# Performance work log

Hardware: AMD Instinct MI355X
Metric: run time of the kernel (lower is better)

The kernel has to match this reference:

```python
import jax, jax.numpy as jnp
import numpy as np

KERNEL = 5
STRIDE = 1
D = 32
B = 8
L = 2048


def setup_inputs() -> dict:
    key = jax.random.key(0)
    k1, k2, k3, k4, k5 = jax.random.split(key, 5)
    dd = D * D
    scale_dense = 1.0 / np.sqrt(dd)
    scale_attn = 1.0 / np.sqrt(dd * KERNEL)
    return {
        "inputs": jax.random.normal(k1, (B, L, D, D), dtype=jnp.float32),
        "W_dense": jax.random.normal(k2, (dd, dd), dtype=jnp.float32) * scale_dense,
        "b_dense": jax.random.normal(k3, (dd,), dtype=jnp.float32) * scale_dense,
        "W_attn": jax.random.normal(k4, (KERNEL, dd * KERNEL), dtype=jnp.float32) * scale_attn,
        "b_attn": jax.random.normal(k5, (KERNEL,), dtype=jnp.float32) * scale_attn,
    }


def _forward(inputs, W_dense, b_dense, W_attn, b_attn):
    b, l, d, _ = inputs.shape
    pad = KERNEL - 1
    pad_left, pad_right = pad // 2, (pad - 1) // 2 + 1

    # Linear2D: linear over flattened d*d dims
    h = jnp.einsum('blde,fe->bldf',
                   inputs.reshape(b, l, d * d)[..., None, :].squeeze(-2).reshape(b, l, 1, d * d),
                   W_dense).reshape(b, l, d * d) + b_dense
    h = h.reshape(b, l, d, d)

    # pad_identity: pad seq dim with identity matrices (neutral for matrix chain)
    eye = jnp.broadcast_to(jnp.eye(d, dtype=inputs.dtype), (b, 1, d, d))
    h_pad = jnp.concatenate(
        [jnp.broadcast_to(eye, (b, pad_left, d, d)), h,
         jnp.broadcast_to(eye, (b, pad_right, d, d))], axis=1)

    out_len = (l + pad - KERNEL) // STRIDE + 1
    # unfold(dim=1, size=KERNEL, step=STRIDE) -> [b, out_len, d, d, KERNEL]
    h_unf = jnp.stack([h_pad[:, k * 1: k + out_len * STRIDE: STRIDE][:, :out_len]
                       for k in range(KERNEL)], axis=-1)

    attention_inputs = h_unf.reshape(b, out_len, d * d * KERNEL)
    scores = attention_inputs @ W_attn.T + b_attn          # [b, out_len, KERNEL]
    alpha = jax.nn.softmax(jax.nn.leaky_relu(scores, 0.01), axis=2)
    alpha = alpha.reshape(b, out_len, 1, 1, KERNEL)

    h_attn = alpha * h_unf                                  # [b, out_len, d, d, KERNEL]
    out = h_attn[..., 0]
    for i in range(1, KERNEL):
        out = jnp.einsum('bcij,bcjk->bcik', out, h_attn[..., i])
    return out


def reference(inputs, W_dense, b_dense, W_attn, b_attn):
    return _forward(inputs, W_dense, b_dense, W_attn, b_attn)
```

## Files before the change

kernel.cpp:

```cpp
#include <hip/hip_runtime.h>
#include <stdint.h>

typedef float  f32x4  __attribute__((ext_vector_type(4)));
typedef float  f32x16 __attribute__((ext_vector_type(16)));
typedef short  s16x8  __attribute__((ext_vector_type(8)));
typedef unsigned short u16x4 __attribute__((ext_vector_type(4)));

#define LPAD 2052

__device__ __forceinline__ float bf2f(unsigned short u){
  unsigned v = ((unsigned)u) << 16;
  return __builtin_bit_cast(float, v);
}
__device__ __forceinline__ unsigned short f2bf(float f){
  unsigned u = __builtin_bit_cast(unsigned, f);
  u += 0x7fffu + ((u >> 16) & 1u);
  return (unsigned short)(u >> 16);
}
__device__ __forceinline__ unsigned cvt_pk_bf16(float lo, float hi){
  unsigned r;
  asm volatile("v_cvt_pk_bf16_f32 %0, %1, %2" : "=v"(r) : "v"(lo), "v"(hi));
  return r;
}

__global__ void k_cvtx(const float* __restrict__ src, unsigned short* __restrict__ dst){
  int b = blockIdx.x;
  int bb = (b & 7) * 2048 + (b >> 3);
  int i = bb * 256 + threadIdx.x;
  f32x4 v = ((const f32x4*)src)[i];
  u16x4 o;
  o[0] = f2bf(v[0]); o[1] = f2bf(v[1]); o[2] = f2bf(v[2]); o[3] = f2bf(v[3]);
  ((u16x4*)dst)[i] = o;
}

__global__ void k_cvt(const float* __restrict__ src, unsigned short* __restrict__ dst, int n4){
  int i = blockIdx.x * 256 + threadIdx.x;
  if (i >= n4) return;
  f32x4 v = ((const f32x4*)src)[i];
  u16x4 o;
  o[0] = f2bf(v[0]); o[1] = f2bf(v[1]); o[2] = f2bf(v[2]); o[3] = f2bf(v[3]);
  ((u16x4*)dst)[i] = o;
}

__global__ void k_eye(unsigned short* __restrict__ H){
  int t = blockIdx.x * 256 + threadIdx.x;
  int b = t >> 12;
  int r = t & 4095;
  int which = r >> 10;
  int ij = r & 1023;
  int p = (which < 2) ? which : (2048 + which);
  H[((size_t)(b * LPAD + p) << 10) + ij] = ((ij >> 5) == (ij & 31)) ? 0x3F80 : 0;
}

__global__ void k_wprep(const float* __restrict__ Wa, unsigned short* __restrict__ Wa2g){
  int t = blockIdx.x * 256 + threadIdx.x;
  int col = t >> 10, e = t & 1023;
  int f = col / 5, kk = col - 5 * f;
  unsigned short v = 0;
  if (col < 25) v = f2bf(Wa[f * 5120 + e * 5 + kk]);
  Wa2g[t] = v;
}

#define MFMA16 __builtin_amdgcn_mfma_f32_16x16x32_bf16

__global__ __launch_bounds__(512, 2) void k_gemm8(const unsigned short* __restrict__ A,
                                                  const unsigned short* __restrict__ Bw,
                                                  const float* __restrict__ bias,
                                                  unsigned short* __restrict__ H){
  __shared__ __align__(128) unsigned short lds[65536];
  const int tid = threadIdx.x;
  const int wid = tid >> 6, l = tid & 63;
  const int wm2 = wid >> 2, wn2 = wid & 3;
  const int lm = l & 15, lk = l >> 4;
  const int hb = blockIdx.x;
  const int xcd = hb & 7, sl = hb >> 3;
  const int bm = xcd * 8 + (sl >> 2), bn = sl & 3;
  const int M0 = bm * 256, N0 = bn * 256;

  const unsigned ko0 = (unsigned)((lk ^ (lm & 7)) << 4);
  const unsigned ko1 = ko0 ^ 64u;
  const unsigned aB0 = (unsigned)wm2 * 16384;
  const unsigned bB0 = 32768u + (unsigned)(wn2 >> 1) * 16384;
  const unsigned rB  = (((unsigned)(wn2 & 1)) * 64 + lm) * 128;
  const unsigned rA  = (unsigned)lm * 128;

  f32x4 acc[8][4] = {};
  s16x8 af[4][2], bf0[2][2], bf1[2][2];

  #define STAGE_HALF(panelRow, mat, bufbase)                                         \
    { _Pragma("unroll")                                                              \
      for (int j = 0; j < 2; j++){                                                   \
        unsigned d = (unsigned)(j * 512 + tid) * 16;                                 \
        unsigned row = d >> 7;                                                       \
        unsigned srcC = ((d >> 4) & 7u) ^ (row & 7u);                                \
        const unsigned short* g = (mat) + (size_t)((panelRow) + row) * 1024          \
                                  + ktK + srcC * 8;                                  \
        __builtin_amdgcn_global_load_lds(                                            \
          (const __attribute__((address_space(1))) void*)g,                          \
          (__attribute__((address_space(3))) void*)&lds[((bufbase) + d) >> 1],       \
          16, 0, 0);                                                                 \
      } }
  #define STAGE_Q(b, kt, q)                                                          \
    { const int ktK = (kt) * 64;                                                     \
      if ((q) == 0)      STAGE_HALF(M0,       A,  (b)*65536u)                        \
      else if ((q) == 1) STAGE_HALF(M0+128,   A,  (b)*65536u+16384u)                 \
      else if ((q) == 2) STAGE_HALF(N0,       Bw, (b)*65536u+32768u)                 \
      else               STAGE_HALF(N0+128,   Bw, (b)*65536u+49152u) }

  #define RD_A(mh) { _Pragma("unroll")                                               \
    for (int m = 0; m < 4; m++){                                                     \
      af[m][0] = *(const s16x8*)&lds[(aB + rA + ((mh)*4+m)*2048u + ko0) >> 1];       \
      af[m][1] = *(const s16x8*)&lds[(aB + rA + ((mh)*4+m)*2048u + ko1) >> 1]; } }
  #define RD_B(dst, nh) { _Pragma("unroll")                                          \
    for (int n = 0; n < 2; n++){                                                     \
      dst[n][0] = *(const s16x8*)&lds[(bB + rB + ((nh)*2+n)*2048u + ko0) >> 1];      \
      dst[n][1] = *(const s16x8*)&lds[(bB + rB + ((nh)*2+n)*2048u + ko1) >> 1]; } }
  #define MM(mo, no, bfr) { _Pragma("unroll")                                        \
    for (int m = 0; m < 4; m++){ _Pragma("unroll")                                   \
      for (int n = 0; n < 2; n++){                                                   \
        acc[(mo)+m][(no)+n] = MFMA16(af[m][0], bfr[n][0], acc[(mo)+m][(no)+n], 0,0,0); \
        acc[(mo)+m][(no)+n] = MFMA16(af[m][1], bfr[n][1], acc[(mo)+m][(no)+n], 0,0,0); } } }
  #define BARA    { __builtin_amdgcn_s_barrier(); asm volatile("s_waitcnt lgkmcnt(0)":::"memory"); __builtin_amdgcn_sched_barrier(0); }
  #define BARA_NL { __builtin_amdgcn_s_barrier(); __builtin_amdgcn_sched_barrier(0); }
  #define BARB    { __builtin_amdgcn_s_barrier(); __builtin_amdgcn_sched_barrier(0); }

  STAGE_Q(0, 0, 0); STAGE_Q(0, 0, 1); STAGE_Q(0, 0, 2); STAGE_Q(0, 0, 3);
  __builtin_amdgcn_sched_barrier(0);
  STAGE_Q(1, 1, 0);
  __builtin_amdgcn_sched_barrier(0);
  asm volatile("s_waitcnt vmcnt(2)" ::: "memory");
  __builtin_amdgcn_s_barrier();
  __builtin_amdgcn_sched_barrier(0);

  #pragma unroll 1
  for (int i = 0; i < 8; i++){
    const int ktA = 2 * i + 1;
    const int ktB = 2 * i + 2;
    const int ktC = 2 * i + 3;
    unsigned aB = aB0, bB = bB0;
    RD_A(0); RD_B(bf0, 0);
    STAGE_Q(1, ktA, 1); STAGE_Q(1, ktA, 2);
    BARA; __builtin_amdgcn_s_setprio(1); MM(0, 0, bf0); __builtin_amdgcn_s_setprio(0); BARB;
    RD_B(bf1, 1);
    STAGE_Q(1, ktA, 3);
    BARA; __builtin_amdgcn_s_setprio(1); MM(0, 2, bf1); __builtin_amdgcn_s_setprio(0); BARB;
    RD_A(1);
    if (ktB < 16) STAGE_Q(0, ktB, 0);
    BARA; __builtin_amdgcn_s_setprio(1); MM(4, 2, bf1); __builtin_amdgcn_s_setprio(0); BARB;
    BARA_NL; __builtin_amdgcn_s_setprio(1); MM(4, 0, bf0); __builtin_amdgcn_s_setprio(0);
    if (i == 7) { asm volatile("s_waitcnt vmcnt(0)" ::: "memory"); }
    else        { asm volatile("s_waitcnt vmcnt(2)" ::: "memory"); }
    BARB;
    aB = 65536u + aB0; bB = 65536u + bB0;
    RD_A(0); RD_B(bf0, 0);
    if (ktB < 16){ STAGE_Q(0, ktB, 1); STAGE_Q(0, ktB, 2); }
    BARA; __builtin_amdgcn_s_setprio(1); MM(0, 0, bf0); __builtin_amdgcn_s_setprio(0); BARB;
    RD_B(bf1, 1);
    if (ktB < 16) STAGE_Q(0, ktB, 3);
    BARA; __builtin_amdgcn_s_setprio(1); MM(0, 2, bf1); __builtin_amdgcn_s_setprio(0); BARB;
    RD_A(1);
    if (ktC < 16) STAGE_Q(1, ktC, 0);
    BARA; __builtin_amdgcn_s_setprio(1); MM(4, 2, bf1); __builtin_amdgcn_s_setprio(0); BARB;
    BARA_NL; __builtin_amdgcn_s_setprio(1); MM(4, 0, bf0); __builtin_amdgcn_s_setprio(0);
    if (i < 7) { asm volatile("s_waitcnt vmcnt(2)" ::: "memory"); }
    BARB;
  }

  float bv[4];
  #pragma unroll
  for (int n = 0; n < 4; n++) bv[n] = bias[N0 + wn2 * 64 + n * 16 + lm];
  #pragma unroll
  for (int m = 0; m < 8; m++){
    #pragma unroll
    for (int r = 0; r < 4; r++){
      int gm = M0 + wm2 * 128 + m * 16 + lk * 4 + r;
      int bb = gm >> 11, li = gm & 2047;
      unsigned short* orow = H + ((size_t)(bb * LPAD + 2 + li) << 10);
      #pragma unroll
      for (int n = 0; n < 4; n++){
        orow[N0 + wn2 * 64 + n * 16 + lm] = f2bf(acc[m][n][r] + bv[n]);
      }
    }
  }
  #undef STAGE_HALF
  #undef STAGE_Q
  #undef RD_A
  #undef RD_B
  #undef MM
  #undef BARA
  #undef BARA_NL
  #undef BARB
}

__global__ __launch_bounds__(256) void k_part(const unsigned short* __restrict__ H,
                                              const unsigned short* __restrict__ Wa2g,
                                              float* __restrict__ part){
  __shared__ unsigned short sB[32768];
  const int tid = threadIdx.x;
  const int wv = tid >> 6, l = tid & 63;
  const int lm = l & 15, lk = l >> 4;
  #pragma unroll
  for (int j = 0; j < 16; j++){
    unsigned d = (unsigned)(j * 256 + tid) * 16;
    unsigned col = d >> 11;
    unsigned srcC = ((d >> 4) & 127u) ^ (col & 7u);
    const unsigned short* g = Wa2g + col * 1024 + srcC * 8;
    __builtin_amdgcn_global_load_lds((const __attribute__((address_space(1))) void*)g,
                                     (__attribute__((address_space(3))) void*)&sB[d >> 1],
                                     16, 0, 0);
  }
  __syncthreads();
  const int rbase = blockIdx.x * 128 + wv * 32;
  f32x4 acc[2][2] = {};
  for (int kk = 0; kk < 1024; kk += 32){
    s16x8 aF[2], bF[2];
    #pragma unroll
    for (int m = 0; m < 2; m++)
      aF[m] = *(const s16x8*)(H + (size_t)(rbase + m * 16 + lm) * 1024 + kk + lk * 8);
    #pragma unroll
    for (int n = 0; n < 2; n++){
      unsigned col = (unsigned)(n * 16 + lm);
      unsigned c = (unsigned)(kk >> 3) + (unsigned)lk;
      bF[n] = *(const s16x8*)&sB[(col * 2048u + ((c ^ (col & 7u)) << 4)) >> 1];
    }
    #pragma unroll
    for (int m = 0; m < 2; m++){
      #pragma unroll
      for (int n = 0; n < 2; n++)
        acc[m][n] = MFMA16(aF[m], bF[n], acc[m][n], 0, 0, 0);
    }
  }
  #pragma unroll
  for (int m = 0; m < 2; m++){
    #pragma unroll
    for (int r = 0; r < 4; r++){
      int row = rbase + m * 16 + lk * 4 + r;
      #pragma unroll
      for (int n = 0; n < 2; n++)
        part[(size_t)row * 32 + n * 16 + lm] = acc[m][n][r];
    }
  }
}

__global__ __launch_bounds__(256) void k_chain(const unsigned short* __restrict__ H,
                                               const float* __restrict__ part,
                                               const float* __restrict__ battn,
                                               float* __restrict__ out){
  const int tid = threadIdx.x;
  const int w = tid >> 6, l = tid & 63;
  const int blk = (blockIdx.x & 7) * 512 + (blockIdx.x >> 3);
  const int pos = blk * 4 + w;
  const int bb = pos >> 11, li = pos & 2047;
  const unsigned short* hbase = H + ((size_t)(bb * LPAD + li) << 10);
  const int col = l & 31;
  const int kh = (l >> 5) << 3;

  const float* prow = part + (size_t)(bb * LPAD + li) * 32;
  float sc[5];
  #pragma unroll
  for (int f = 0; f < 5; f++){
    float a = battn[f];
    #pragma unroll
    for (int k = 0; k < 5; k++)
      a += prow[k * 32 + f * 5 + k];
    sc[f] = (a > 0.f) ? a : 0.01f * a;
  }
  float mx = sc[0];
  #pragma unroll
  for (int f = 1; f < 5; f++) mx = fmaxf(mx, sc[f]);
  float e0 = expf(sc[0] - mx), e1 = expf(sc[1] - mx), e2 = expf(sc[2] - mx),
        e3 = expf(sc[3] - mx), e4 = expf(sc[4] - mx);
  float ssum = e0 + e1 + e2 + e3 + e4;
  float inv = 1.f / ssum;
  float inv2 = inv * inv;
  const float sv = (e0 * e1 * e2 * e3 * e4) * inv2 * inv2 * inv;

  const unsigned short* h4 = hbase + 4 * 1024;
  unsigned q0, q1, q2, q3, q4, q5, q6, q7;
  {
    #define LD2(kk) ((unsigned)h4[(kk) * 32 + col] | ((unsigned)h4[((kk) + 1) * 32 + col] << 16))
    q0 = LD2(kh + 0);  q1 = LD2(kh + 2);  q2 = LD2(kh + 4);  q3 = LD2(kh + 6);
    q4 = LD2(kh + 16); q5 = LD2(kh + 18); q6 = LD2(kh + 20); q7 = LD2(kh + 22);
    #undef LD2
  }
  union { unsigned u[4]; s16x8 v; } ub0, ub1;
  ub0.u[0] = q0; ub0.u[1] = q1; ub0.u[2] = q2; ub0.u[3] = q3;
  ub1.u[0] = q4; ub1.u[1] = q5; ub1.u[2] = q6; ub1.u[3] = q7;
  s16x8 Bf0 = ub0.v, Bf1 = ub1.v;

  f32x16 acc;
  #pragma unroll
  for (int st = 0; st < 4; st++){
    const int km = 3 - st;
    const unsigned short* hA = hbase + (km << 10);
    s16x8 A0 = *(const s16x8*)(hA + col * 32 + kh);
    s16x8 A1 = *(const s16x8*)(hA + col * 32 + kh + 16);
    f32x16 z = {0,0,0,0,0,0,0,0,0,0,0,0,0,0,0,0};
    acc = __builtin_amdgcn_mfma_f32_32x32x16_bf16(A0, Bf0, z,   0, 0, 0);
    acc = __builtin_amdgcn_mfma_f32_32x32x16_bf16(A1, Bf1, acc, 0, 0, 0);
    if (st < 3){
      unsigned d0 = cvt_pk_bf16(acc[0],  acc[1]);
      unsigned d1 = cvt_pk_bf16(acc[2],  acc[3]);
      unsigned d2 = cvt_pk_bf16(acc[4],  acc[5]);
      unsigned d3 = cvt_pk_bf16(acc[6],  acc[7]);
      unsigned d4 = cvt_pk_bf16(acc[8],  acc[9]);
      unsigned d5 = cvt_pk_bf16(acc[10], acc[11]);
      unsigned d6 = cvt_pk_bf16(acc[12], acc[13]);
      unsigned d7 = cvt_pk_bf16(acc[14], acc[15]);
      unsigned p0 = __shfl_xor(d0, 32, 64);
      unsigned p1 = __shfl_xor(d1, 32, 64);
      unsigned p2 = __shfl_xor(d2, 32, 64);
      unsigned p3 = __shfl_xor(d3, 32, 64);
      unsigned p4 = __shfl_xor(d4, 32, 64);
      unsigned p5 = __shfl_xor(d5, 32, 64);
      unsigned p6 = __shfl_xor(d6, 32, 64);
      unsigned p7 = __shfl_xor(d7, 32, 64);
      const bool lo = (l < 32);
      ub0.u[0] = lo ? d0 : p2;  ub0.u[1] = lo ? d1 : p3;
      ub0.u[2] = lo ? p0 : d2;  ub0.u[3] = lo ? p1 : d3;
      ub1.u[0] = lo ? d4 : p6;  ub1.u[1] = lo ? d5 : p7;
      ub1.u[2] = lo ? p4 : d6;  ub1.u[3] = lo ? p5 : d7;
      Bf0 = ub0.v; Bf1 = ub1.v;
    }
  }

  float* ob = out + ((size_t)pos << 10);
  #pragma unroll
  for (int t = 0; t < 16; t++){
    int row = (t & 3) + 8 * (t >> 2) + ((l >> 5) << 2);
    ob[row * 32 + col] = sv * acc[t];
  }
}

extern "C" void kernel_launch(void* const* d_in, const int* in_sizes, int n_in,
                              void* d_out, int out_size, void* d_ws, size_t ws_size,
                              hipStream_t stream){
  const float* X  = (const float*)d_in[0];
  const float* Wd = (const float*)d_in[1];
  const float* bd = (const float*)d_in[2];
  const float* Wa = (const float*)d_in[3];
  const float* ba = (const float*)d_in[4];
  float* out = (float*)d_out;

  char* ws = (char*)d_ws;
  unsigned short* Hpad = (unsigned short*)ws;
  unsigned short* Wbf  = (unsigned short*)(ws + 33619968);
  unsigned short* Wa2g = (unsigned short*)(ws + 33619968 + 2097152);
  float*          part = (float*)(ws + 33619968 + 2097152 + 65536);
  unsigned short* Xbf  = (unsigned short*)d_out;

  k_cvtx<<<16384, 256, 0, stream>>>(X, Xbf);
  k_cvt<<<1024, 256, 0, stream>>>(Wd, Wbf, 262144);
  k_eye<<<128, 256, 0, stream>>>(Hpad);
  k_wprep<<<128, 256, 0, stream>>>(Wa, Wa2g);
  k_gemm8<<<256, 512, 0, stream>>>(Xbf, Wbf, bd, Hpad);
  k_part<<<129, 256, 0, stream>>>(Hpad, Wa2g, part);
  k_chain<<<4096, 256, 0, stream>>>(Hpad, part, ba, out);
}
```

Baseline: 94.58 us.

## Replace pipelined 256x256 GEMM with simpler single-buffered 256x128 tile kernel

Replaces the hand-scheduled double-buffered 256x256-tile dense GEMM with a plain single-buffer 256x128-tile kernel using 4x4 MFMA per wave and syncthreads around each k-step. This doubles the grid to 512 blocks and cuts LDS per block, allowing higher occupancy (launch bounds 4). It gives up the explicit load/compute overlap, interleaved barriers and priority tricks, so global-to-LDS latency is exposed within each block and must be hidden by other resident blocks.

```diff
diff --git a/kernel.cpp b/kernel.cpp
--- a/kernel.cpp
+++ b/kernel.cpp
@@ -63,133 +63,89 @@
 
 #define MFMA16 __builtin_amdgcn_mfma_f32_16x16x32_bf16
 
-__global__ __launch_bounds__(512, 2) void k_gemm8(const unsigned short* __restrict__ A,
+__global__ __launch_bounds__(512, 4) void k_gemm2(const unsigned short* __restrict__ A,
                                                   const unsigned short* __restrict__ Bw,
                                                   const float* __restrict__ bias,
                                                   unsigned short* __restrict__ H){
-  __shared__ __align__(128) unsigned short lds[65536];
+  __shared__ __align__(128) unsigned short lds[24576];
   const int tid = threadIdx.x;
   const int wid = tid >> 6, l = tid & 63;
-  const int wm2 = wid >> 2, wn2 = wid & 3;
+  const int wm = wid >> 1, wn = wid & 1;
   const int lm = l & 15, lk = l >> 4;
   const int hb = blockIdx.x;
   const int xcd = hb & 7, sl = hb >> 3;
-  const int bm = xcd * 8 + (sl >> 2), bn = sl & 3;
-  const int M0 = bm * 256, N0 = bn * 256;
+  const int bm = xcd * 8 + (sl >> 3), bn = sl & 7;
+  const int M0 = bm * 256, N0 = bn * 128;
 
   const unsigned ko0 = (unsigned)((lk ^ (lm & 7)) << 4);
   const unsigned ko1 = ko0 ^ 64u;
-  const unsigned aB0 = (unsigned)wm2 * 16384;
-  const unsigned bB0 = 32768u + (unsigned)(wn2 >> 1) * 16384;
-  const unsigned rB  = (((unsigned)(wn2 & 1)) * 64 + lm) * 128;
-  const unsigned rA  = (unsigned)lm * 128;
-
-  f32x4 acc[8][4] = {};
-  s16x8 af[4][2], bf0[2][2], bf1[2][2];
-
-  #define STAGE_HALF(panelRow, mat, bufbase)                                         \
-    { _Pragma("unroll")                                                              \
-      for (int j = 0; j < 2; j++){                                                   \
-        unsigned d = (unsigned)(j * 512 + tid) * 16;                                 \
-        unsigned row = d >> 7;                                                       \
-        unsigned srcC = ((d >> 4) & 7u) ^ (row & 7u);                                \
-        const unsigned short* g = (mat) + (size_t)((panelRow) + row) * 1024          \
-                                  + ktK + srcC * 8;                                  \
-        __builtin_amdgcn_global_load_lds(                                            \
-          (const __attribute__((address_space(1))) void*)g,                          \
-          (__attribute__((address_space(3))) void*)&lds[((bufbase) + d) >> 1],       \
-          16, 0, 0);                                                                 \
-      } }
-  #define STAGE_Q(b, kt, q)                                                          \
-    { const int ktK = (kt) * 64;                                                     \
-      if ((q) == 0)      STAGE_HALF(M0,       A,  (b)*65536u)                        \
-      else if ((q) == 1) STAGE_HALF(M0+128,   A,  (b)*65536u+16384u)                 \
-      else if ((q) == 2) STAGE_HALF(N0,       Bw, (b)*65536u+32768u)                 \
-      else               STAGE_HALF(N0+128,   Bw, (b)*65536u+49152u) }
-
-  #define RD_A(mh) { _Pragma("unroll")                                               \
-    for (int m = 0; m < 4; m++){                                                     \
-      af[m][0] = *(const s16x8*)&lds[(aB + rA + ((mh)*4+m)*2048u + ko0) >> 1];       \
-      af[m][1] = *(const s16x8*)&lds[(aB + rA + ((mh)*4+m)*2048u + ko1) >> 1]; } }
-  #define RD_B(dst, nh) { _Pragma("unroll")                                          \
-    for (int n = 0; n < 2; n++){                                                     \
-      dst[n][0] = *(const s16x8*)&lds[(bB + rB + ((nh)*2+n)*2048u + ko0) >> 1];      \
-      dst[n][1] = *(const s16x8*)&lds[(bB + rB + ((nh)*2+n)*2048u + ko1) >> 1]; } }
-  #define MM(mo, no, bfr) { _Pragma("unroll")                                        \
-    for (int m = 0; m < 4; m++){ _Pragma("unroll")                                   \
-      for (int n = 0; n < 2; n++){                                                   \
-        acc[(mo)+m][(no)+n] = MFMA16(af[m][0], bfr[n][0], acc[(mo)+m][(no)+n], 0,0,0); \
-        acc[(mo)+m][(no)+n] = MFMA16(af[m][1], bfr[n][1], acc[(mo)+m][(no)+n], 0,0,0); } } }
-  #define BARA    { __builtin_amdgcn_s_barrier(); asm volatile("s_waitcnt lgkmcnt(0)":::"memory"); __builtin_amdgcn_sched_barrier(0); }
-  #define BARA_NL { __builtin_amdgcn_s_barrier(); __builtin_amdgcn_sched_barrier(0); }
-  #define BARB    { __builtin_amdgcn_s_barrier(); __builtin_amdgcn_sched_barrier(0); }
-
-  STAGE_Q(0, 0, 0); STAGE_Q(0, 0, 1); STAGE_Q(0, 0, 2); STAGE_Q(0, 0, 3);
-  __builtin_amdgcn_sched_barrier(0);
-  STAGE_Q(1, 1, 0);
-  __builtin_amdgcn_sched_barrier(0);
-  asm volatile("s_waitcnt vmcnt(2)" ::: "memory");
-  __builtin_amdgcn_s_barrier();
-  __builtin_amdgcn_sched_barrier(0);
-
-  #pragma unroll 1
-  for (int i = 0; i < 8; i++){
-    const int ktA = 2 * i + 1;
-    const int ktB = 2 * i + 2;
-    const int ktC = 2 * i + 3;
-    unsigned aB = aB0, bB = bB0;
-    RD_A(0); RD_B(bf0, 0);
-    STAGE_Q(1, ktA, 1); STAGE_Q(1, ktA, 2);
-    BARA; __builtin_amdgcn_s_setprio(1); MM(0, 0, bf0); __builtin_amdgcn_s_setprio(0); BARB;
-    RD_B(bf1, 1);
-    STAGE_Q(1, ktA, 3);
-    BARA; __builtin_amdgcn_s_setprio(1); MM(0, 2, bf1); __builtin_amdgcn_s_setprio(0); BARB;
-    RD_A(1);
-    if (ktB < 16) STAGE_Q(0, ktB, 0);
-    BARA; __builtin_amdgcn_s_setprio(1); MM(4, 2, bf1); __builtin_amdgcn_s_setprio(0); BARB;
-    BARA_NL; __builtin_amdgcn_s_setprio(1); MM(4, 0, bf0); __builtin_amdgcn_s_setprio(0);
-    if (i == 7) { asm volatile("s_waitcnt vmcnt(0)" ::: "memory"); }
-    else        { asm volatile("s_waitcnt vmcnt(2)" ::: "memory"); }
-    BARB;
-    aB = 65536u + aB0; bB = 65536u + bB0;
-    RD_A(0); RD_B(bf0, 0);
-    if (ktB < 16){ STAGE_Q(0, ktB, 1); STAGE_Q(0, ktB, 2); }
-    BARA; __builtin_amdgcn_s_setprio(1); MM(0, 0, bf0); __builtin_amdgcn_s_setprio(0); BARB;
-    RD_B(bf1, 1);
-    if (ktB < 16) STAGE_Q(0, ktB, 3);
-    BARA; __builtin_amdgcn_s_setprio(1); MM(0, 2, bf1); __builtin_amdgcn_s_setprio(0); BARB;
-    RD_A(1);
-    if (ktC < 16) STAGE_Q(1, ktC, 0);
-    BARA; __builtin_amdgcn_s_setprio(1); MM(4, 2, bf1); __builtin_amdgcn_s_setprio(0); BARB;
-    BARA_NL; __builtin_amdgcn_s_setprio(1); MM(4, 0, bf0); __builtin_amdgcn_s_setprio(0);
-    if (i < 7) { asm volatile("s_waitcnt vmcnt(2)" ::: "memory"); }
-    BARB;
+  const unsigned rA = ((unsigned)(wm * 64 + lm)) * 128u;
+  const unsigned rB = 32768u + ((unsigned)(wn * 64 + lm)) * 128u;
+
+  f32x4 acc[4][4] = {};
+
+  for (int kt = 0; kt < 16; ++kt){
+    const int ktK = kt * 64;
+    #pragma unroll
+    for (int j = 0; j < 6; j++){
+      unsigned d = (unsigned)(j * 512 + tid) * 16;
+      const unsigned short* g;
+      if (j < 4){
+        unsigned row = d >> 7;
+        unsigned srcC = ((d >> 4) & 7u) ^ (row & 7u);
+        g = A + (size_t)(M0 + row) * 1024 + ktK + srcC * 8;
+      } else {
+        unsigned db = d - 32768u;
+        unsigned row = db >> 7;
+        unsigned srcC = ((db >> 4) & 7u) ^ (row & 7u);
+        g = Bw + (size_t)(N0 + row) * 1024 + ktK + srcC * 8;
+      }
+      __builtin_amdgcn_global_load_lds((const __attribute__((address_space(1))) void*)g,
+                                       (__attribute__((address_space(3))) void*)&lds[d >> 1],
+                                       16, 0, 0);
+    }
+    __syncthreads();
+
+    s16x8 a0[4], b0[4];
+    #pragma unroll
+    for (int m = 0; m < 4; m++) a0[m] = *(const s16x8*)&lds[(rA + m * 2048u + ko0) >> 1];
+    #pragma unroll
+    for (int n = 0; n < 4; n++) b0[n] = *(const s16x8*)&lds[(rB + n * 2048u + ko0) >> 1];
+    #pragma unroll
+    for (int m = 0; m < 4; m++){
+      #pragma unroll
+      for (int n = 0; n < 4; n++)
+        acc[m][n] = MFMA16(a0[m], b0[n], acc[m][n], 0, 0, 0);
+    }
+    #pragma unroll
+    for (int m = 0; m < 4; m++) a0[m] = *(const s16x8*)&lds[(rA + m * 2048u + ko1) >> 1];
+    #pragma unroll
+    for (int n = 0; n < 4; n++) b0[n] = *(const s16x8*)&lds[(rB + n * 2048u + ko1) >> 1];
+    #pragma unroll
+    for (int m = 0; m < 4; m++){
+      #pragma unroll
+      for (int n = 0; n < 4; n++)
+        acc[m][n] = MFMA16(a0[m], b0[n], acc[m][n], 0, 0, 0);
+    }
+    __syncthreads();
   }
 
   float bv[4];
   #pragma unroll
-  for (int n = 0; n < 4; n++) bv[n] = bias[N0 + wn2 * 64 + n * 16 + lm];
-  #pragma unroll
-  for (int m = 0; m < 8; m++){
+  for (int n = 0; n < 4; n++) bv[n] = bias[N0 + wn * 64 + n * 16 + lm];
+  #pragma unroll
+  for (int m = 0; m < 4; m++){
     #pragma unroll
     for (int r = 0; r < 4; r++){
-      int gm = M0 + wm2 * 128 + m * 16 + lk * 4 + r;
+      int gm = M0 + wm * 64 + m * 16 + lk * 4 + r;
       int bb = gm >> 11, li = gm & 2047;
       unsigned short* orow = H + ((size_t)(bb * LPAD + 2 + li) << 10);
       #pragma unroll
       for (int n = 0; n < 4; n++){
-        orow[N0 + wn2 * 64 + n * 16 + lm] = f2bf(acc[m][n][r] + bv[n]);
+        orow[N0 + wn * 64 + n * 16 + lm] = f2bf(acc[m][n][r] + bv[n]);
       }
     }
   }
-  #undef STAGE_HALF
-  #undef STAGE_Q
-  #undef RD_A
-  #undef RD_B
-  #undef MM
-  #undef BARA
-  #undef BARA_NL
-  #undef BARB
 }
 
 __global__ __launch_bounds__(256) void k_part(const unsigned short* __restrict__ H,
@@ -353,7 +309,7 @@
   k_cvt<<<1024, 256, 0, stream>>>(Wd, Wbf, 262144);
   k_eye<<<128, 256, 0, stream>>>(Hpad);
   k_wprep<<<128, 256, 0, stream>>>(Wa, Wa2g);
-  k_gemm8<<<256, 512, 0, stream>>>(Xbf, Wbf, bd, Hpad);
+  k_gemm2<<<512, 512, 0, stream>>>(Xbf, Wbf, bd, Hpad);
   k_part<<<129, 256, 0, stream>>>(Hpad, Wa2g, part);
   k_chain<<<4096, 256, 0, stream>>>(Hpad, part, ba, out);
 }
```

Measured after the change: 94.53 us. Within noise of the previous version (-0.0%).
